# Performance work log

Hardware: AMD Instinct MI355X
Metric: run time of the kernel (lower is better)

Reference implementation:

```python
import jax, jax.numpy as jnp
import numpy as np

B, N, D = 2, 2048, 1024
H, DH = 16, 64
DI = 4096
EPS = 1e-5
NEG_SLOPE = 0.01  # F.leaky_relu default


def _ln(x, g, b):
    mu = jnp.mean(x, axis=-1, keepdims=True)
    var = jnp.mean((x - mu) ** 2, axis=-1, keepdims=True)
    return (x - mu) * jax.lax.rsqrt(var + EPS) * g + b


def setup_inputs() -> dict:
    key = jax.random.key(0)
    ks = jax.random.split(key, 10)
    s = 0.02
    return {
        "Z": jax.random.normal(ks[0], (B, N, D), jnp.float32),
        "new_mask": jax.random.normal(ks[1], (B, N, N), jnp.float32),
        "mask": jax.random.uniform(ks[2], (B, N, N), jnp.float32),
        "ln1_g": jnp.ones((D,), jnp.float32),
        "ln1_b": jnp.zeros((D,), jnp.float32),
        "qkv_w": jax.random.normal(ks[3], (3 * D, D), jnp.float32) * s,
        "qkv_b": jnp.zeros((3 * D,), jnp.float32),
        "o_w": jax.random.normal(ks[4], (D, H * DH), jnp.float32) * s,
        "ln2_g": jnp.ones((D,), jnp.float32),
        "ln2_b": jnp.zeros((D,), jnp.float32),
        "p1_w": jax.random.normal(ks[5], (DI, D), jnp.float32) * s,
        "p1_b": jnp.zeros((DI,), jnp.float32),
        "p2_w": jax.random.normal(ks[6], (D, DI), jnp.float32) * s,
        "p2_b": jnp.zeros((D,), jnp.float32),
    }


def reference(Z, new_mask, mask, ln1_g, ln1_b, qkv_w, qkv_b, o_w, ln2_g, ln2_b, p1_w, p1_b, p2_w, p2_b):
    inp = Z
    Zn = _ln(Z, ln1_g, ln1_b)
    qkv = (Zn @ qkv_w.T + qkv_b).reshape(B, N, H, 3 * DH)
    # torch chunk order in the source: V, Q, K
    V, Q, K = jnp.split(qkv, 3, axis=3)  # each [B,N,H,DH]
    # scores: einsum('bnij,bmij->binm') == [B,H,N,N]
    W = jnp.einsum("bnhd,bmhd->bhnm", Q, K) / np.sqrt(DH) + new_mask[:, None]
    A = jax.nn.softmax(W, axis=3) * mask[:, None]
    attn = jnp.einsum("bhnm,bmhd->bnhd", A, V).reshape(B, N, D)
    attn = jnp.where(attn >= 0, attn, NEG_SLOPE * attn) @ o_w.T  # leaky_relu then o_net (no bias)
    Z1 = attn + inp
    Zn2 = _ln(Z1, ln2_g, ln2_b)
    h = jax.nn.relu(Zn2 @ p1_w.T + p1_b)
    return h @ p2_w.T + p2_b + Z1
```

## Files before the change

kernel.cpp:

```cpp
#include <hip/hip_runtime.h>

typedef unsigned short u16;
typedef __attribute__((ext_vector_type(8))) short bf16x8;
typedef __attribute__((ext_vector_type(2))) float f32x2;
typedef __attribute__((ext_vector_type(4))) float f32x4;
typedef __attribute__((ext_vector_type(16))) float f32x16;
typedef __attribute__((ext_vector_type(4))) unsigned u32x4;

#define DEV static __device__ __forceinline__

DEV u16 f2bf(float f) {
    unsigned u = __float_as_uint(f);
    u += 0x7FFFu + ((u >> 16) & 1u);
    return (u16)(u >> 16);
}

DEV float uaf(unsigned u) { return __uint_as_float(u); }

typedef const __attribute__((address_space(1))) void* gas1_t;
typedef __attribute__((address_space(3))) void* gas3_t;

DEV void gl_lds16(const u16* g, u16* l) {
    __builtin_amdgcn_global_load_lds((gas1_t)g, (gas3_t)l, 16, 0, 0);
}

DEV unsigned cvtpk_bf16(float a, float b) {
    unsigned r;
    asm("v_cvt_pk_bf16_f32 %0, %1, %2" : "=v"(r) : "v"(a), "v"(b));
    return r;
}

DEV int sw8(int row, int chunk) { return row * 64 + ((chunk ^ (row & 7)) << 3); }

__global__ __launch_bounds__(256) void prep_all(const float* __restrict__ qkv_w,
                                                const float* __restrict__ o_w,
                                                const float* __restrict__ p1_w,
                                                const float* __restrict__ p2_w,
                                                const float* __restrict__ qkv_b,
                                                const float* __restrict__ nm,
                                                const float* __restrict__ pm,
                                                const float* __restrict__ Z,
                                                const float* __restrict__ ln1_g,
                                                const float* __restrict__ ln1_b,
                                                u16* __restrict__ qkvW,
                                                u16* __restrict__ oW,
                                                u16* __restrict__ p1W,
                                                u16* __restrict__ p2W,
                                                float* __restrict__ pbias,
                                                unsigned* __restrict__ Mp,
                                                u16* __restrict__ Zn) {
    __shared__ uint4 Ls[512];
    __shared__ float rs[4], rss[4];
    const int bid = blockIdx.x, t = threadIdx.x;
    if (bid < 3072) {
        int i = bid * 256 + t;
        int orow = i >> 8, cc = i & 255;
        int region = orow >> 10, rem = orow & 1023, h = rem >> 6, tt = rem & 63;
        int srow = h * 192 + region * 64 + tt;
        float4 v = ((const float4*)qkv_w)[srow * 256 + cc];
        ushort4 o;
        o.x = f2bf(v.x); o.y = f2bf(v.y); o.z = f2bf(v.z); o.w = f2bf(v.w);
        ((ushort4*)qkvW)[i] = o;
    } else if (bid < 4096) {
        int i = (bid - 3072) * 256 + t;
        float4 v = ((const float4*)o_w)[i];
        ushort4 o;
        o.x = f2bf(v.x); o.y = f2bf(v.y); o.z = f2bf(v.z); o.w = f2bf(v.w);
        ((ushort4*)oW)[i] = o;
    } else if (bid < 8192) {
        int i = (bid - 4096) * 256 + t;
        float4 v = ((const float4*)p1_w)[i];
        ushort4 o;
        o.x = f2bf(v.x); o.y = f2bf(v.y); o.z = f2bf(v.z); o.w = f2bf(v.w);
        ((ushort4*)p1W)[i] = o;
    } else if (bid < 12288) {
        int i = (bid - 8192) * 256 + t;
        float4 v = ((const float4*)p2_w)[i];
        ushort4 o;
        o.x = f2bf(v.x); o.y = f2bf(v.y); o.z = f2bf(v.z); o.w = f2bf(v.w);
        ((ushort4*)p2W)[i] = o;
    } else if (bid < 16384) {
        const int idx = bid - 12288;
        const int bb = idx >> 11, r2 = idx & 2047;
        const int mt = r2 >> 5, nt = r2 & 31;
        const int n0 = nt * 64;
        const int n = t >> 2;
        const int mq0 = (t & 3) * 2;
        const size_t fbase = (size_t)bb * 1048576 + (size_t)(n0 + n) * 512 + mt * 8 + mq0;
        const float4 a0 = ((const float4*)nm)[fbase];
        const float4 a1 = ((const float4*)nm)[fbase + 1];
        const float4 b0 = ((const float4*)pm)[fbase];
        const float4 b1 = ((const float4*)pm)[fbase + 1];
        uint4 o0, o1;
        o0.x = ((unsigned)f2bf(b0.x) << 16) | f2bf(a0.x * 1.4426950f);
        o0.y = ((unsigned)f2bf(b0.y) << 16) | f2bf(a0.y * 1.4426950f);
        o0.z = ((unsigned)f2bf(b0.z) << 16) | f2bf(a0.z * 1.4426950f);
        o0.w = ((unsigned)f2bf(b0.w) << 16) | f2bf(a0.w * 1.4426950f);
        o1.x = ((unsigned)f2bf(b1.x) << 16) | f2bf(a1.x * 1.4426950f);
        o1.y = ((unsigned)f2bf(b1.y) << 16) | f2bf(a1.y * 1.4426950f);
        o1.z = ((unsigned)f2bf(b1.z) << 16) | f2bf(a1.z * 1.4426950f);
        o1.w = ((unsigned)f2bf(b1.w) << 16) | f2bf(a1.w * 1.4426950f);
        const int c = mq0 >> 1;
        Ls[c * 128 + n * 2 + 0] = o0;
        Ls[c * 128 + n * 2 + 1] = o1;
        __syncthreads();
        const int wc = t >> 6, j = t & 63;
        const size_t obase = (((size_t)(bb * 64 + mt) * 4) + wc) * 4096 + (size_t)n0 * 2;
        ((uint4*)Mp)[obase + j] = Ls[wc * 128 + j];
        ((uint4*)Mp)[obase + 64 + j] = Ls[wc * 128 + 64 + j];
    } else if (bid < 20480) {
        const int row = bid - 16384;
        const float4 v = ((const float4*)(Z + (size_t)row * 1024))[t];
        float s = v.x + v.y + v.z + v.w;
        float ss = v.x * v.x + v.y * v.y + v.z * v.z + v.w * v.w;
#pragma unroll
        for (int o = 1; o < 64; o <<= 1) {
            s += __shfl_xor(s, o);
            ss += __shfl_xor(ss, o);
        }
        const int wave = t >> 6, lane = t & 63;
        if (lane == 0) { rs[wave] = s; rss[wave] = ss; }
        __syncthreads();
        const float tot = rs[0] + rs[1] + rs[2] + rs[3];
        const float totss = rss[0] + rss[1] + rss[2] + rss[3];
        const float mu = tot * (1.0f / 1024.0f);
        const float var = totss * (1.0f / 1024.0f) - mu * mu;
        const float rstd = rsqrtf(var + 1e-5f);
        const float4 g4 = ((const float4*)ln1_g)[t];
        const float4 b4 = ((const float4*)ln1_b)[t];
        ushort4 o;
        o.x = f2bf((v.x - mu) * rstd * g4.x + b4.x);
        o.y = f2bf((v.y - mu) * rstd * g4.y + b4.y);
        o.z = f2bf((v.z - mu) * rstd * g4.z + b4.z);
        o.w = f2bf((v.w - mu) * rstd * g4.w + b4.w);
        ((ushort4*)(Zn + (size_t)row * 1024))[t] = o;
    } else {
#pragma unroll
        for (int k = 0; k < 12; k++) {
            int i = k * 256 + t;
            int region = i >> 10, rem = i & 1023, h = rem >> 6, tt = rem & 63;
            pbias[i] = qkv_b[h * 192 + region * 64 + tt];
        }
    }
}

__global__ __launch_bounds__(256) void ln2_comb2(const float* __restrict__ p0,
                                                 const float* __restrict__ p1,
                                                 const float* __restrict__ Z,
                                                 const float* __restrict__ gam,
                                                 const float* __restrict__ bet,
                                                 float* __restrict__ Z1,
                                                 u16* __restrict__ y) {
    const int row = blockIdx.x;
    const int t = threadIdx.x;
    const size_t off = (size_t)row * 256 + t;
    const float4 a = ((const float4*)p0)[off];
    const float4 c = ((const float4*)p1)[off];
    const float4 z = ((const float4*)Z)[off];
    float4 v;
    v.x = a.x + c.x + z.x;
    v.y = a.y + c.y + z.y;
    v.z = a.z + c.z + z.z;
    v.w = a.w + c.w + z.w;
    ((float4*)Z1)[off] = v;
    float s = v.x + v.y + v.z + v.w;
    float ss = v.x * v.x + v.y * v.y + v.z * v.z + v.w * v.w;
#pragma unroll
    for (int o = 1; o < 64; o <<= 1) {
        s += __shfl_xor(s, o);
        ss += __shfl_xor(ss, o);
    }
    __shared__ float rs[4], rss[4];
    const int wave = t >> 6, lane = t & 63;
    if (lane == 0) { rs[wave] = s; rss[wave] = ss; }
    __syncthreads();
    const float tot = rs[0] + rs[1] + rs[2] + rs[3];
    const float totss = rss[0] + rss[1] + rss[2] + rss[3];
    const float mu = tot * (1.0f / 1024.0f);
    const float var = totss * (1.0f / 1024.0f) - mu * mu;
    const float rstd = rsqrtf(var + 1e-5f);
    const float4 g4 = ((const float4*)gam)[t];
    const float4 b4 = ((const float4*)bet)[t];
    ushort4 o;
    o.x = f2bf((v.x - mu) * rstd * g4.x + b4.x);
    o.y = f2bf((v.y - mu) * rstd * g4.y + b4.y);
    o.z = f2bf((v.z - mu) * rstd * g4.z + b4.z);
    o.w = f2bf((v.w - mu) * rstd * g4.w + b4.w);
    ((ushort4*)(y + (size_t)row * 1024))[t] = o;
}

__global__ __launch_bounds__(256) void out_comb(const float* __restrict__ p0,
                                                const float* __restrict__ p1,
                                                const float* __restrict__ bias,
                                                const float* __restrict__ Z1,
                                                float* __restrict__ out) {
    int i = blockIdx.x * 256 + threadIdx.x;
    float4 a = ((const float4*)p0)[i];
    float4 c = ((const float4*)p1)[i];
    float4 z = ((const float4*)Z1)[i];
    float4 b = ((const float4*)bias)[i & 255];
    float4 o;
    o.x = a.x + c.x + z.x + b.x; o.y = a.y + c.y + z.y + b.y;
    o.z = a.z + c.z + z.z + b.z; o.w = a.w + c.w + z.w + b.w;
    ((float4*)out)[i] = o;
}

template <int EPI>
__global__ __launch_bounds__(256, 3) void gemm_bt(const u16* __restrict__ A,
                                                  const u16* __restrict__ Bt,
                                                  const float* __restrict__ bias,
                                                  void* __restrict__ out0,
                                                  void* __restrict__ out1,
                                                  void* __restrict__ out2,
                                                  int M, int N, int K, int ldk) {
    __shared__ __align__(16) u16 As[2][128 * 32];
    __shared__ __align__(16) u16 Bs[2][128 * 32];
    const int tid = threadIdx.x;
    const int wave = tid >> 6, lane = tid & 63;
    const int lhi = lane >> 4, llo = lane & 15;
    const int gx = gridDim.x;
    const int bid = blockIdx.y * gx + blockIdx.x;
    const int swz = (bid & 7) * ((gx * gridDim.y) >> 3) + (bid >> 3);
    const int bx = swz % gx, by = swz / gx;
    const int kz = blockIdx.z * K;

    const int arow = wave * 32 + (lane >> 2);
    const int asw = ((lane & 3) ^ ((lane >> 2) & 3)) << 3;
    const u16* gA = A + (size_t)(by * 128 + arow) * ldk + kz + asw;
    const u16* gB = Bt + (size_t)(bx * 128 + arow) * ldk + kz + asw;
    u16* lA0 = As[0] + wave * 1024 + lane * 8;
    u16* lA1 = As[1] + wave * 1024 + lane * 8;
    u16* lB0 = Bs[0] + wave * 1024 + lane * 8;
    u16* lB1 = Bs[1] + wave * 1024 + lane * 8;

#define GSTAGE(LA, LB) do { \
        gl_lds16(gA, LA); gl_lds16(gA + 16 * (size_t)ldk, (LA) + 512); \
        gl_lds16(gB, LB); gl_lds16(gB + 16 * (size_t)ldk, (LB) + 512); \
        gA += 32; gB += 32; } while (0)

    const int wr = wave >> 1, wc = wave & 1;
    const f32x4 zero = {0.f, 0.f, 0.f, 0.f};
    f32x4 acc[4][4];
#pragma unroll
    for (int i = 0; i < 4; i++)
#pragma unroll
        for (int j = 0; j < 4; j++) acc[i][j] = zero;

#define GPHASE(AB, BB, DO_REFILL, LA, LB, LASTWAIT) do { \
        if (LASTWAIT) asm volatile("s_waitcnt vmcnt(0)" ::: "memory"); \
        else          asm volatile("s_waitcnt vmcnt(4)" ::: "memory"); \
        __builtin_amdgcn_s_barrier(); \
        bf16x8 af[4], bfr[4]; \
        _Pragma("unroll") \
        for (int i = 0; i < 4; i++) { \
            const int r = wr * 64 + i * 16 + llo; \
            af[i] = *(const bf16x8*)((AB) + r * 32 + (((lhi ^ r) & 3) << 3)); \
        } \
        _Pragma("unroll") \
        for (int j = 0; j < 4; j++) { \
            const int r = wc * 64 + j * 16 + llo; \
            bfr[j] = *(const bf16x8*)((BB) + r * 32 + (((lhi ^ r) & 3) << 3)); \
        } \
        asm volatile("s_waitcnt lgkmcnt(0)" ::: "memory"); \
        __builtin_amdgcn_sched_barrier(0); \
        __builtin_amdgcn_s_barrier(); \
        if (DO_REFILL) GSTAGE(LA, LB); \
        __builtin_amdgcn_s_setprio(1); \
        _Pragma("unroll") \
        for (int i = 0; i < 4; i++) \
            _Pragma("unroll") \
            for (int j = 0; j < 4; j++) \
                acc[i][j] = __builtin_amdgcn_mfma_f32_16x16x32_bf16(af[i], bfr[j], acc[i][j], 0, 0, 0); \
        __builtin_amdgcn_s_setprio(0); \
        } while (0)

    GSTAGE(lA0, lB0);
    GSTAGE(lA1, lB1);
    for (int k0 = 0; k0 < K; k0 += 64) {
        const bool r0 = (k0 + 64 < K);
        const bool r1 = (k0 + 96 < K);
        GPHASE(As[0], Bs[0], r0, lA0, lB0, false);
        GPHASE(As[1], Bs[1], r1, lA1, lB1, !r0);
    }
#undef GPHASE
#undef GSTAGE

    const int rbase = by * 128 + wr * 64 + lhi * 4;
    const int cbase = bx * 128 + wc * 64 + llo;
    float* pout = nullptr;
    if constexpr (EPI == 4) {
        pout = (float*)out0 + (size_t)blockIdx.z * M * N;
    }
#pragma unroll
    for (int i = 0; i < 4; i++) {
#pragma unroll
        for (int j = 0; j < 4; j++) {
#pragma unroll
            for (int r = 0; r < 4; r++) {
                const int row = rbase + i * 16 + r;
                const int col = cbase + j * 16;
                float v = acc[i][j][r];
                if constexpr (EPI == 0) {
                    v += bias[col];
                    const int region = col >> 10;
                    const int c = col & 1023;
                    const int b = row >> 11, n = row & 2047;
                    if (region == 0) {
                        ((float*)out0)[(size_t)row * 1024 + c] = v;
                    } else {
                        const int h = c >> 6, t = c & 63;
                        u16* dst = (region == 1) ? (u16*)out1 : (u16*)out2;
                        dst[(((size_t)(b * 16 + h)) * 2048 + n) * 64 + t] = f2bf(v);
                    }
                } else if constexpr (EPI == 2) {
                    v += bias[col];
                    v = v > 0.f ? v : 0.f;
                    ((u16*)out0)[(size_t)row * N + col] = f2bf(v);
                } else {
                    pout[(size_t)row * N + col] = v;
                }
            }
        }
    }
}

__global__ __launch_bounds__(256) void vtrans(const float* __restrict__ Vsc,
                                              u16* __restrict__ Vt) {
    __shared__ u16 Ts[64 * 72];
    const int nt = blockIdx.x;
    const int bh = blockIdx.y;
    const int b = bh >> 4, h = bh & 15;
    const int t = threadIdx.x;
    const int n0 = nt * 64;
    const int nr = t >> 2;
    const int dq = (t & 3) * 16;
    const float* src = Vsc + ((size_t)(b * 2048 + n0 + nr)) * 1024 + h * 64 + dq;
    float4 v0 = ((const float4*)src)[0];
    float4 v1 = ((const float4*)src)[1];
    float4 v2 = ((const float4*)src)[2];
    float4 v3 = ((const float4*)src)[3];
    u16* c0 = Ts + nr;
    c0[(dq + 0) * 72]  = f2bf(v0.x); c0[(dq + 1) * 72]  = f2bf(v0.y);
    c0[(dq + 2) * 72]  = f2bf(v0.z); c0[(dq + 3) * 72]  = f2bf(v0.w);
    c0[(dq + 4) * 72]  = f2bf(v1.x); c0[(dq + 5) * 72]  = f2bf(v1.y);
    c0[(dq + 6) * 72]  = f2bf(v1.z); c0[(dq + 7) * 72]  = f2bf(v1.w);
    c0[(dq + 8) * 72]  = f2bf(v2.x); c0[(dq + 9) * 72]  = f2bf(v2.y);
    c0[(dq + 10) * 72] = f2bf(v2.z); c0[(dq + 11) * 72] = f2bf(v2.w);
    c0[(dq + 12) * 72] = f2bf(v3.x); c0[(dq + 13) * 72] = f2bf(v3.y);
    c0[(dq + 14) * 72] = f2bf(v3.z); c0[(dq + 15) * 72] = f2bf(v3.w);
    __syncthreads();
    const int d = t >> 2, n8 = (t & 3) * 16;
    u16* dstrow = Vt + ((size_t)bh * 64 + d) * 2048 + n0;
#pragma unroll
    for (int w = 0; w < 4; w++) {
        const int gi = (n8 >> 2) + w;
        const int g5 = gi & 7, blk = gi >> 3;
        const int pg = (g5 & 4) | ((g5 & 1) << 1) | ((g5 >> 1) & 1);
        *(uint2*)(dstrow + blk * 32 + pg * 4) = *(const uint2*)(Ts + d * 72 + n8 + w * 4);
    }
}

__global__ __launch_bounds__(256, 4) void attn_fused8(const u16* __restrict__ Qg,
                                                      const u16* __restrict__ Kg,
                                                      const u16* __restrict__ Vtg,
                                                      const unsigned* __restrict__ Mp,
                                                      u16* __restrict__ attnL) {
    __shared__ __align__(16) u16 Ks[2][64 * 64];
    __shared__ __align__(16) u16 Vs[2][64 * 64];
    __shared__ float lsh[2][32], lsh2[2][32];
    const int tid = threadIdx.x, wave = tid >> 6, lane = tid & 63;
    const int qh = wave & 1, wm = wave >> 1;
    const int hi = lane >> 5, l31 = lane & 31;
    const int pid = blockIdx.x;
    const int seq = pid >> 3;
    const int hh = seq & 15;
    const int g = (pid & 7) + (seq >> 4) * 8;
    const int b = g >> 5, qt = g & 31;
    const int bh = b * 16 + hh;
    const int q0 = qt * 64;

    const int l3 = lane >> 3, l7 = lane & 7;
    const int swcol = (l7 ^ l3) << 3;
    const int srow = wave * 16 + l3;
    const u16* kp = Kg + ((size_t)bh * 2048 + srow) * 64 + swcol;
    const u16* vp = Vtg + ((size_t)bh * 64 + srow) * 2048 + swcol;
    u16* lKa = Ks[0] + wave * 1024 + lane * 8;
    u16* lKb = Ks[1] + wave * 1024 + lane * 8;
    u16* lVa = Vs[0] + wave * 1024 + lane * 8;
    u16* lVb = Vs[1] + wave * 1024 + lane * 8;

#define STAGE(LK, LV) do { \
        gl_lds16(kp, LK); gl_lds16(kp + 512, (LK) + 512); \
        gl_lds16(vp, LV); gl_lds16(vp + 16384, (LV) + 512); \
        kp += 4096; vp += 64; } while (0)

    STAGE(lKa, lVa);
    const int qrow = q0 + qh * 32 + l31;
    const u16* qptr = Qg + ((size_t)bh * 2048 + qrow) * 64 + hi * 8;
    bf16x8 qf[4];
#pragma unroll
    for (int ks = 0; ks < 4; ks++) qf[ks] = *(const bf16x8*)(qptr + ks * 16);

    const uint4* mp = (const uint4*)Mp + (size_t)(b * 64 + wm) * 16384
                                       + (size_t)qrow * 2 + hi;

    const f32x16 z16 = {0.f,0.f,0.f,0.f,0.f,0.f,0.f,0.f,0.f,0.f,0.f,0.f,0.f,0.f,0.f,0.f};
    f32x16 accO[2];
    accO[0] = z16; accO[1] = z16;
    f32x2 lsv = {0.f, 0.f};
    const float CS = 0.125f * 1.4426950f;
    const f32x2 csv = {CS, CS};
    __syncthreads();

#define QUAD(M, q) { \
        f32x2 nm0 = {uaf(M.x << 16), uaf(M.y << 16)}; \
        f32x2 nm1 = {uaf(M.z << 16), uaf(M.w << 16)}; \
        const f32x2 sa = {sacc[q], sacc[q + 1]}; \
        const f32x2 sb = {sacc[q + 2], sacc[q + 3]}; \
        nm0 += sa * csv; nm1 += sb * csv; \
        f32x2 e0 = {__builtin_amdgcn_exp2f(nm0.x), __builtin_amdgcn_exp2f(nm0.y)}; \
        f32x2 e1 = {__builtin_amdgcn_exp2f(nm1.x), __builtin_amdgcn_exp2f(nm1.y)}; \
        lsv += e0; lsv += e1; \
        const f32x2 pm0 = {uaf(M.x & 0xFFFF0000u), uaf(M.y & 0xFFFF0000u)}; \
        const f32x2 pm1 = {uaf(M.z & 0xFFFF0000u), uaf(M.w & 0xFFFF0000u)}; \
        e0 *= pm0; e1 *= pm1; \
        wpk[(q) / 2] = cvtpk_bf16(e0.x, e0.y); \
        wpk[(q) / 2 + 1] = cvtpk_bf16(e1.x, e1.y); }

#define ITER(KSB, VSB, LK, LV, DO_STAGE) do { \
        const uint4 M0 = mp[0], M1 = mp[4096], M2 = mp[8192], M3 = mp[12288]; \
        mp += 32768; \
        if (DO_STAGE) STAGE(LK, LV); \
        f32x16 sacc = z16; \
        __builtin_amdgcn_s_setprio(1); \
        _Pragma("unroll") \
        for (int ks = 0; ks < 4; ks++) { \
            const bf16x8 kf = *(const bf16x8*)((KSB) + sw8(wm * 32 + l31, ks * 2 + hi)); \
            sacc = __builtin_amdgcn_mfma_f32_32x32x16_bf16(kf, qf[ks], sacc, 0, 0, 0); \
        } \
        __builtin_amdgcn_s_setprio(0); \
        unsigned wpk[8]; \
        QUAD(M0, 0) QUAD(M1, 4) QUAD(M2, 8) QUAD(M3, 12) \
        const u32x4 fa0v = {wpk[0], wpk[1], wpk[2], wpk[3]}; \
        const u32x4 fa1v = {wpk[4], wpk[5], wpk[6], wpk[7]}; \
        const bf16x8 pa0 = __builtin_bit_cast(bf16x8, fa0v); \
        const bf16x8 pa1 = __builtin_bit_cast(bf16x8, fa1v); \
        __builtin_amdgcn_s_setprio(1); \
        _Pragma("unroll") \
        for (int dh = 0; dh < 2; dh++) { \
            const bf16x8 vf0 = *(const bf16x8*)((VSB) + sw8(dh * 32 + l31, wm * 4 + hi)); \
            accO[dh] = __builtin_amdgcn_mfma_f32_32x32x16_bf16(pa0, vf0, accO[dh], 0, 0, 0); \
            const bf16x8 vf1 = *(const bf16x8*)((VSB) + sw8(dh * 32 + l31, wm * 4 + 2 + hi)); \
            accO[dh] = __builtin_amdgcn_mfma_f32_32x32x16_bf16(pa1, vf1, accO[dh], 0, 0, 0); \
        } \
        __builtin_amdgcn_s_setprio(0); \
        __syncthreads(); } while (0)

    for (int tt = 0; tt < 16; tt++) {
        ITER(Ks[0], Vs[0], lKb, lVb, true);
        ITER(Ks[1], Vs[1], lKa, lVa, (tt < 15));
    }
#undef ITER
#undef QUAD
#undef STAGE

    const float lsum = lsv.x + lsv.y;
    const float lsum2 = lsum + __shfl_xor(lsum, 32);
    float* cb = (float*)&Ks[0][0];
    const int slot = qh * 64 + lane;
    const int s7 = slot & 7;
    if (wm == 1) {
        float* dst = cb + (size_t)slot * 32;
#pragma unroll
        for (int dh = 0; dh < 2; dh++)
#pragma unroll
            for (int c = 0; c < 4; c++) {
                const f32x4 v = {accO[dh][c * 4 + 0], accO[dh][c * 4 + 1],
                                 accO[dh][c * 4 + 2], accO[dh][c * 4 + 3]};
                *(f32x4*)(dst + (((dh * 4 + c) ^ s7) << 2)) = v;
            }
        if (lane < 32) lsh[qh][lane] = lsum2;
    }
    __syncthreads();
    if (wm == 0) {
        const float* src = cb + (size_t)slot * 32;
        const float lt = lsum2 + lsh[qh][l31];
#pragma unroll
        for (int dh = 0; dh < 2; dh++)
#pragma unroll
            for (int c = 0; c < 4; c++) {
                const f32x4 v = *(const f32x4*)(src + (((dh * 4 + c) ^ s7) << 2));
                accO[dh][c * 4 + 0] += v.x;
                accO[dh][c * 4 + 1] += v.y;
                accO[dh][c * 4 + 2] += v.z;
                accO[dh][c * 4 + 3] += v.w;
            }
        if (lane < 32) lsh2[qh][lane] = 1.0f / lt;
    }
    __syncthreads();
    if (wm == 0) {
#pragma unroll
        for (int r = 0; r < 16; r++) {
            const int ql = (r & 3) + 8 * (r >> 2) + 4 * hi;
            const float linv = lsh2[qh][ql];
            const int qg = q0 + qh * 32 + ql;
#pragma unroll
            for (int dh = 0; dh < 2; dh++) {
                float v = accO[dh][r] * linv;
                v = v >= 0.f ? v : 0.01f * v;
                attnL[((size_t)b * 2048 + qg) * 1024 + hh * 64 + dh * 32 + l31] = f2bf(v);
            }
        }
    }
}

extern "C" void kernel_launch(void* const* d_in, const int* in_sizes, int n_in,
                              void* d_out, int out_size, void* d_ws, size_t ws_size,
                              hipStream_t stream) {
    const float* Z     = (const float*)d_in[0];
    const float* nmask = (const float*)d_in[1];
    const float* pmask = (const float*)d_in[2];
    const float* ln1_g = (const float*)d_in[3];
    const float* ln1_b = (const float*)d_in[4];
    const float* qkv_w = (const float*)d_in[5];
    const float* qkv_b = (const float*)d_in[6];
    const float* o_w   = (const float*)d_in[7];
    const float* ln2_g = (const float*)d_in[8];
    const float* ln2_b = (const float*)d_in[9];
    const float* p1_w  = (const float*)d_in[10];
    const float* p1_b  = (const float*)d_in[11];
    const float* p2_w  = (const float*)d_in[12];
    const float* p2_b  = (const float*)d_in[13];
    float* out = (float*)d_out;

    char* w = (char*)d_ws;
    auto take = [&](size_t bytes) -> char* {
        char* p = w;
        w += (bytes + 255) & ~(size_t)255;
        return p;
    };
    u16* qkvW   = (u16*)take((size_t)3072 * 1024 * 2);
    u16* oW     = (u16*)take((size_t)1024 * 1024 * 2);
    u16* p1W    = (u16*)take((size_t)4096 * 1024 * 2);
    u16* p2W    = (u16*)take((size_t)1024 * 4096 * 2);
    u16* Zn     = (u16*)take((size_t)4096 * 1024 * 2);
    u16* Qb     = (u16*)take((size_t)32 * 2048 * 64 * 2);
    u16* Kb     = (u16*)take((size_t)32 * 2048 * 64 * 2);
    u16* Vt     = (u16*)take((size_t)32 * 64 * 2048 * 2);
    u16* attnL  = (u16*)take((size_t)4096 * 1024 * 2);
    float* Z1   = (float*)take((size_t)4096 * 1024 * 4);
    u16* hbuf   = (u16*)take((size_t)4096 * 4096 * 2);
    unsigned* Mp = (unsigned*)take((size_t)2 * 2048 * 2048 * 4);
    float* pbias = (float*)take((size_t)3072 * 4);
    float* Vsc    = (float*)hbuf;
    float* part01 = (float*)Mp;
    float* part23 = (float*)hbuf;

    prep_all<<<dim3(20481), 256, 0, stream>>>(qkv_w, o_w, p1_w, p2_w, qkv_b, nmask, pmask,
                                              Z, ln1_g, ln1_b,
                                              qkvW, oW, p1W, p2W, pbias, Mp, Zn);
    gemm_bt<0><<<dim3(24, 32), 256, 0, stream>>>(Zn, qkvW, pbias, Vsc, Qb, Kb, 4096, 3072, 1024, 1024);
    vtrans<<<dim3(32, 32), 256, 0, stream>>>(Vsc, Vt);
    attn_fused8<<<dim3(1024), 256, 0, stream>>>(Qb, Kb, Vt, Mp, attnL);
    gemm_bt<4><<<dim3(8, 32, 2), 256, 0, stream>>>(attnL, oW, nullptr, part01, nullptr, nullptr,
                                                   4096, 1024, 512, 1024);
    ln2_comb2<<<dim3(4096), 256, 0, stream>>>(part01, part01 + (size_t)4096 * 1024,
                                              Z, ln2_g, ln2_b, Z1, Zn);
    gemm_bt<2><<<dim3(32, 32), 256, 0, stream>>>(Zn, p1W, p1_b, hbuf, nullptr, nullptr,
                                                 4096, 4096, 1024, 1024);
    gemm_bt<4><<<dim3(8, 32, 2), 256, 0, stream>>>(hbuf, p2W, nullptr, part01, nullptr, nullptr,
                                                   4096, 1024, 2048, 4096);
    out_comb<<<dim3(4096), 256, 0, stream>>>(part01, part01 + (size_t)4096 * 1024, p2_b, Z1, out);
}
```

Baseline: 407.6 us.

## Prefetch mask tiles one iteration ahead and fold additive mask into MFMA accumulator

The attention kernel now loads the packed mask tile for the next key block one iteration early, using double-buffered registers, so global-load latency overlaps the current block's compute. The additive mask is pre-scaled by 8 in the prep kernel and written into the score accumulator as its initial value, so the MFMA adds it for free. The whole sum is then multiplied by the combined softmax and log2e scale before exp2. This adds register pressure from the extra 16 mask words held per thread, and changes bf16 rounding of the mask because it is stored scaled by 8 instead of by log2e.

```diff
diff --git a/kernel.cpp b/kernel.cpp
--- a/kernel.cpp
+++ b/kernel.cpp
@@ -92,14 +92,14 @@
         const float4 b0 = ((const float4*)pm)[fbase];
         const float4 b1 = ((const float4*)pm)[fbase + 1];
         uint4 o0, o1;
-        o0.x = ((unsigned)f2bf(b0.x) << 16) | f2bf(a0.x * 1.4426950f);
-        o0.y = ((unsigned)f2bf(b0.y) << 16) | f2bf(a0.y * 1.4426950f);
-        o0.z = ((unsigned)f2bf(b0.z) << 16) | f2bf(a0.z * 1.4426950f);
-        o0.w = ((unsigned)f2bf(b0.w) << 16) | f2bf(a0.w * 1.4426950f);
-        o1.x = ((unsigned)f2bf(b1.x) << 16) | f2bf(a1.x * 1.4426950f);
-        o1.y = ((unsigned)f2bf(b1.y) << 16) | f2bf(a1.y * 1.4426950f);
-        o1.z = ((unsigned)f2bf(b1.z) << 16) | f2bf(a1.z * 1.4426950f);
-        o1.w = ((unsigned)f2bf(b1.w) << 16) | f2bf(a1.w * 1.4426950f);
+        o0.x = ((unsigned)f2bf(b0.x) << 16) | f2bf(a0.x * 8.0f);
+        o0.y = ((unsigned)f2bf(b0.y) << 16) | f2bf(a0.y * 8.0f);
+        o0.z = ((unsigned)f2bf(b0.z) << 16) | f2bf(a0.z * 8.0f);
+        o0.w = ((unsigned)f2bf(b0.w) << 16) | f2bf(a0.w * 8.0f);
+        o1.x = ((unsigned)f2bf(b1.x) << 16) | f2bf(a1.x * 8.0f);
+        o1.y = ((unsigned)f2bf(b1.y) << 16) | f2bf(a1.y * 8.0f);
+        o1.z = ((unsigned)f2bf(b1.z) << 16) | f2bf(a1.z * 8.0f);
+        o1.w = ((unsigned)f2bf(b1.w) << 16) | f2bf(a1.w * 8.0f);
         const int c = mq0 >> 1;
         Ls[c * 128 + n * 2 + 0] = o0;
         Ls[c * 128 + n * 2 + 1] = o1;
@@ -360,7 +360,7 @@
     }
 }
 
-__global__ __launch_bounds__(256, 4) void attn_fused8(const u16* __restrict__ Qg,
+__global__ __launch_bounds__(256, 4) void attn_fused9(const u16* __restrict__ Qg,
                                                       const u16* __restrict__ Kg,
                                                       const u16* __restrict__ Vtg,
                                                       const unsigned* __restrict__ Mp,
@@ -403,6 +403,9 @@
 
     const uint4* mp = (const uint4*)Mp + (size_t)(b * 64 + wm) * 16384
                                        + (size_t)qrow * 2 + hi;
+    uint4 mA0 = mp[0], mA1 = mp[4096], mA2 = mp[8192], mA3 = mp[12288];
+    uint4 mB0, mB1, mB2, mB3;
+    mp += 32768;
 
     const f32x16 z16 = {0.f,0.f,0.f,0.f,0.f,0.f,0.f,0.f,0.f,0.f,0.f,0.f,0.f,0.f,0.f,0.f};
     f32x16 accO[2];
@@ -413,13 +416,10 @@
     __syncthreads();
 
 #define QUAD(M, q) { \
-        f32x2 nm0 = {uaf(M.x << 16), uaf(M.y << 16)}; \
-        f32x2 nm1 = {uaf(M.z << 16), uaf(M.w << 16)}; \
-        const f32x2 sa = {sacc[q], sacc[q + 1]}; \
-        const f32x2 sb = {sacc[q + 2], sacc[q + 3]}; \
-        nm0 += sa * csv; nm1 += sb * csv; \
-        f32x2 e0 = {__builtin_amdgcn_exp2f(nm0.x), __builtin_amdgcn_exp2f(nm0.y)}; \
-        f32x2 e1 = {__builtin_amdgcn_exp2f(nm1.x), __builtin_amdgcn_exp2f(nm1.y)}; \
+        const f32x2 s0 = {sacc[q] * CS, sacc[q + 1] * CS}; \
+        const f32x2 s1 = {sacc[q + 2] * CS, sacc[q + 3] * CS}; \
+        f32x2 e0 = {__builtin_amdgcn_exp2f(s0.x), __builtin_amdgcn_exp2f(s0.y)}; \
+        f32x2 e1 = {__builtin_amdgcn_exp2f(s1.x), __builtin_amdgcn_exp2f(s1.y)}; \
         lsv += e0; lsv += e1; \
         const f32x2 pm0 = {uaf(M.x & 0xFFFF0000u), uaf(M.y & 0xFFFF0000u)}; \
         const f32x2 pm1 = {uaf(M.z & 0xFFFF0000u), uaf(M.w & 0xFFFF0000u)}; \
@@ -427,11 +427,21 @@
         wpk[(q) / 2] = cvtpk_bf16(e0.x, e0.y); \
         wpk[(q) / 2 + 1] = cvtpk_bf16(e1.x, e1.y); }
 
-#define ITER(KSB, VSB, LK, LV, DO_STAGE) do { \
-        const uint4 M0 = mp[0], M1 = mp[4096], M2 = mp[8192], M3 = mp[12288]; \
-        mp += 32768; \
-        if (DO_STAGE) STAGE(LK, LV); \
-        f32x16 sacc = z16; \
+#define ITER(KSB, VSB, LK, LV, MC0, MC1, MC2, MC3, MN0, MN1, MN2, MN3, DO_PF) do { \
+        if (DO_PF) { \
+            MN0 = mp[0]; MN1 = mp[4096]; MN2 = mp[8192]; MN3 = mp[12288]; \
+            mp += 32768; \
+            STAGE(LK, LV); \
+        } \
+        f32x16 sacc; \
+        sacc[0] = uaf(MC0.x << 16); sacc[1] = uaf(MC0.y << 16); \
+        sacc[2] = uaf(MC0.z << 16); sacc[3] = uaf(MC0.w << 16); \
+        sacc[4] = uaf(MC1.x << 16); sacc[5] = uaf(MC1.y << 16); \
+        sacc[6] = uaf(MC1.z << 16); sacc[7] = uaf(MC1.w << 16); \
+        sacc[8] = uaf(MC2.x << 16); sacc[9] = uaf(MC2.y << 16); \
+        sacc[10] = uaf(MC2.z << 16); sacc[11] = uaf(MC2.w << 16); \
+        sacc[12] = uaf(MC3.x << 16); sacc[13] = uaf(MC3.y << 16); \
+        sacc[14] = uaf(MC3.z << 16); sacc[15] = uaf(MC3.w << 16); \
         __builtin_amdgcn_s_setprio(1); \
         _Pragma("unroll") \
         for (int ks = 0; ks < 4; ks++) { \
@@ -440,7 +450,7 @@
         } \
         __builtin_amdgcn_s_setprio(0); \
         unsigned wpk[8]; \
-        QUAD(M0, 0) QUAD(M1, 4) QUAD(M2, 8) QUAD(M3, 12) \
+        QUAD(MC0, 0) QUAD(MC1, 4) QUAD(MC2, 8) QUAD(MC3, 12) \
         const u32x4 fa0v = {wpk[0], wpk[1], wpk[2], wpk[3]}; \
         const u32x4 fa1v = {wpk[4], wpk[5], wpk[6], wpk[7]}; \
         const bf16x8 pa0 = __builtin_bit_cast(bf16x8, fa0v); \
@@ -457,8 +467,8 @@
         __syncthreads(); } while (0)
 
     for (int tt = 0; tt < 16; tt++) {
-        ITER(Ks[0], Vs[0], lKb, lVb, true);
-        ITER(Ks[1], Vs[1], lKa, lVa, (tt < 15));
+        ITER(Ks[0], Vs[0], lKb, lVb, mA0, mA1, mA2, mA3, mB0, mB1, mB2, mB3, true);
+        ITER(Ks[1], Vs[1], lKa, lVa, mB0, mB1, mB2, mB3, mA0, mA1, mA2, mA3, (tt < 15));
     }
 #undef ITER
 #undef QUAD
@@ -561,7 +571,7 @@
                                               qkvW, oW, p1W, p2W, pbias, Mp, Zn);
     gemm_bt<0><<<dim3(24, 32), 256, 0, stream>>>(Zn, qkvW, pbias, Vsc, Qb, Kb, 4096, 3072, 1024, 1024);
     vtrans<<<dim3(32, 32), 256, 0, stream>>>(Vsc, Vt);
-    attn_fused8<<<dim3(1024), 256, 0, stream>>>(Qb, Kb, Vt, Mp, attnL);
+    attn_fused9<<<dim3(1024), 256, 0, stream>>>(Qb, Kb, Vt, Mp, attnL);
     gemm_bt<4><<<dim3(8, 32, 2), 256, 0, stream>>>(attnL, oW, nullptr, part01, nullptr, nullptr,
                                                    4096, 1024, 512, 1024);
     ln2_comb2<<<dim3(4096), 256, 0, stream>>>(part01, part01 + (size_t)4096 * 1024,
```

After: 453.2 us. +11.2%, slower.

## Fuse V transpose into QKV GEMM epilogue via LDS-staged bf16 stores

Applied to the files above, without the earlier changes.

The QKV GEMM epilogue now writes the V region straight into the transposed, permuted bf16 Vt layout. It stages the tile through the reused LDS buffers with an XOR swizzle and then does 16-byte coalesced stores. This removes the separate vtrans kernel and the fp32 Vsc round trip through global memory. The cost is extra barriers and LDS traffic in the V blocks' epilogue, plus a divergent epilogue path between V blocks and Q/K blocks.

```diff
diff --git a/kernel.cpp b/kernel.cpp
--- a/kernel.cpp
+++ b/kernel.cpp
@@ -213,8 +213,7 @@
                                                   void* __restrict__ out1,
                                                   void* __restrict__ out2,
                                                   int M, int N, int K, int ldk) {
-    __shared__ __align__(16) u16 As[2][128 * 32];
-    __shared__ __align__(16) u16 Bs[2][128 * 32];
+    __shared__ __align__(16) u16 SH[4][128 * 32];
     const int tid = threadIdx.x;
     const int wave = tid >> 6, lane = tid & 63;
     const int lhi = lane >> 4, llo = lane & 15;
@@ -228,10 +227,10 @@
     const int asw = ((lane & 3) ^ ((lane >> 2) & 3)) << 3;
     const u16* gA = A + (size_t)(by * 128 + arow) * ldk + kz + asw;
     const u16* gB = Bt + (size_t)(bx * 128 + arow) * ldk + kz + asw;
-    u16* lA0 = As[0] + wave * 1024 + lane * 8;
-    u16* lA1 = As[1] + wave * 1024 + lane * 8;
-    u16* lB0 = Bs[0] + wave * 1024 + lane * 8;
-    u16* lB1 = Bs[1] + wave * 1024 + lane * 8;
+    u16* lA0 = SH[0] + wave * 1024 + lane * 8;
+    u16* lA1 = SH[1] + wave * 1024 + lane * 8;
+    u16* lB0 = SH[2] + wave * 1024 + lane * 8;
+    u16* lB1 = SH[3] + wave * 1024 + lane * 8;
 
 #define GSTAGE(LA, LB) do { \
         gl_lds16(gA, LA); gl_lds16(gA + 16 * (size_t)ldk, (LA) + 512); \
@@ -279,84 +278,93 @@
     for (int k0 = 0; k0 < K; k0 += 64) {
         const bool r0 = (k0 + 64 < K);
         const bool r1 = (k0 + 96 < K);
-        GPHASE(As[0], Bs[0], r0, lA0, lB0, false);
-        GPHASE(As[1], Bs[1], r1, lA1, lB1, !r0);
+        GPHASE(SH[0], SH[2], r0, lA0, lB0, false);
+        GPHASE(SH[1], SH[3], r1, lA1, lB1, !r0);
     }
 #undef GPHASE
 #undef GSTAGE
 
     const int rbase = by * 128 + wr * 64 + lhi * 4;
     const int cbase = bx * 128 + wc * 64 + llo;
-    float* pout = nullptr;
-    if constexpr (EPI == 4) {
-        pout = (float*)out0 + (size_t)blockIdx.z * M * N;
-    }
-#pragma unroll
-    for (int i = 0; i < 4; i++) {
-#pragma unroll
-        for (int j = 0; j < 4; j++) {
-#pragma unroll
-            for (int r = 0; r < 4; r++) {
-                const int row = rbase + i * 16 + r;
-                const int col = cbase + j * 16;
-                float v = acc[i][j][r];
-                if constexpr (EPI == 0) {
-                    v += bias[col];
-                    const int region = col >> 10;
-                    const int c = col & 1023;
-                    const int b = row >> 11, n = row & 2047;
-                    if (region == 0) {
-                        ((float*)out0)[(size_t)row * 1024 + c] = v;
+    if constexpr (EPI == 0) {
+        if (cbase < 1024) {
+            __syncthreads();
+            u16* T = &SH[0][0];
+#pragma unroll
+            for (int i = 0; i < 4; i++) {
+#pragma unroll
+                for (int r = 0; r < 4; r++) {
+                    const int nl = wr * 64 + lhi * 4 + i * 16 + r;
+                    const int g5 = (nl >> 2) & 7;
+                    const int pg = (g5 & 4) | ((g5 & 1) << 1) | ((g5 >> 1) & 1);
+                    const int slot = (nl & ~31) | (pg << 2) | (nl & 3);
+#pragma unroll
+                    for (int j = 0; j < 4; j++) {
+                        const int d = llo + j * 16;
+                        const float v = acc[i][j][r] + bias[cbase + j * 16];
+                        T[wc * 8192 + d * 128 +
+                          ((((slot >> 3) ^ d) & 15) << 3) + (slot & 7)] = f2bf(v);
+                    }
+                }
+            }
+            __syncthreads();
+            const int rowid = tid >> 1, half = tid & 1;
+            const int h2 = rowid >> 6, dd = rowid & 63;
+            const int bb2 = by >> 4;
+            const int nb = (by & 15) * 128;
+            const int headg = bx * 2 + h2;
+            u16* dst = (u16*)out0 + ((size_t)(bb2 * 16 + headg) * 64 + dd) * 2048
+                                  + nb + half * 64;
+            const u16* srcT = T + h2 * 8192 + dd * 128;
+#pragma unroll
+            for (int k = 0; k < 8; k++) {
+                const int grp = half * 8 + k;
+                ((uint4*)dst)[k] = *(const uint4*)(srcT + (((grp ^ dd) & 15) << 3));
+            }
+        } else {
+#pragma unroll
+            for (int i = 0; i < 4; i++) {
+#pragma unroll
+                for (int j = 0; j < 4; j++) {
+#pragma unroll
+                    for (int r = 0; r < 4; r++) {
+                        const int row = rbase + i * 16 + r;
+                        const int col = cbase + j * 16;
+                        const float v = acc[i][j][r] + bias[col];
+                        const int region = col >> 10;
+                        const int c = col & 1023;
+                        const int b = row >> 11, n = row & 2047;
+                        const int h = c >> 6, t2 = c & 63;
+                        u16* dst = (region == 1) ? (u16*)out1 : (u16*)out2;
+                        dst[(((size_t)(b * 16 + h)) * 2048 + n) * 64 + t2] = f2bf(v);
+                    }
+                }
+            }
+        }
+    } else {
+        float* pout = nullptr;
+        if constexpr (EPI == 4) {
+            pout = (float*)out0 + (size_t)blockIdx.z * M * N;
+        }
+#pragma unroll
+        for (int i = 0; i < 4; i++) {
+#pragma unroll
+            for (int j = 0; j < 4; j++) {
+#pragma unroll
+                for (int r = 0; r < 4; r++) {
+                    const int row = rbase + i * 16 + r;
+                    const int col = cbase + j * 16;
+                    float v = acc[i][j][r];
+                    if constexpr (EPI == 2) {
+                        v += bias[col];
+                        v = v > 0.f ? v : 0.f;
+                        ((u16*)out0)[(size_t)row * N + col] = f2bf(v);
                     } else {
-                        const int h = c >> 6, t = c & 63;
-                        u16* dst = (region == 1) ? (u16*)out1 : (u16*)out2;
-                        dst[(((size_t)(b * 16 + h)) * 2048 + n) * 64 + t] = f2bf(v);
+                        pout[(size_t)row * N + col] = v;
                     }
-                } else if constexpr (EPI == 2) {
-                    v += bias[col];
-                    v = v > 0.f ? v : 0.f;
-                    ((u16*)out0)[(size_t)row * N + col] = f2bf(v);
-                } else {
-                    pout[(size_t)row * N + col] = v;
                 }
             }
         }
-    }
-}
-
-__global__ __launch_bounds__(256) void vtrans(const float* __restrict__ Vsc,
-                                              u16* __restrict__ Vt) {
-    __shared__ u16 Ts[64 * 72];
-    const int nt = blockIdx.x;
-    const int bh = blockIdx.y;
-    const int b = bh >> 4, h = bh & 15;
-    const int t = threadIdx.x;
-    const int n0 = nt * 64;
-    const int nr = t >> 2;
-    const int dq = (t & 3) * 16;
-    const float* src = Vsc + ((size_t)(b * 2048 + n0 + nr)) * 1024 + h * 64 + dq;
-    float4 v0 = ((const float4*)src)[0];
-    float4 v1 = ((const float4*)src)[1];
-    float4 v2 = ((const float4*)src)[2];
-    float4 v3 = ((const float4*)src)[3];
-    u16* c0 = Ts + nr;
-    c0[(dq + 0) * 72]  = f2bf(v0.x); c0[(dq + 1) * 72]  = f2bf(v0.y);
-    c0[(dq + 2) * 72]  = f2bf(v0.z); c0[(dq + 3) * 72]  = f2bf(v0.w);
-    c0[(dq + 4) * 72]  = f2bf(v1.x); c0[(dq + 5) * 72]  = f2bf(v1.y);
-    c0[(dq + 6) * 72]  = f2bf(v1.z); c0[(dq + 7) * 72]  = f2bf(v1.w);
-    c0[(dq + 8) * 72]  = f2bf(v2.x); c0[(dq + 9) * 72]  = f2bf(v2.y);
-    c0[(dq + 10) * 72] = f2bf(v2.z); c0[(dq + 11) * 72] = f2bf(v2.w);
-    c0[(dq + 12) * 72] = f2bf(v3.x); c0[(dq + 13) * 72] = f2bf(v3.y);
-    c0[(dq + 14) * 72] = f2bf(v3.z); c0[(dq + 15) * 72] = f2bf(v3.w);
-    __syncthreads();
-    const int d = t >> 2, n8 = (t & 3) * 16;
-    u16* dstrow = Vt + ((size_t)bh * 64 + d) * 2048 + n0;
-#pragma unroll
-    for (int w = 0; w < 4; w++) {
-        const int gi = (n8 >> 2) + w;
-        const int g5 = gi & 7, blk = gi >> 3;
-        const int pg = (g5 & 4) | ((g5 & 1) << 1) | ((g5 >> 1) & 1);
-        *(uint2*)(dstrow + blk * 32 + pg * 4) = *(const uint2*)(Ts + d * 72 + n8 + w * 4);
     }
 }
 
@@ -552,15 +560,12 @@
     u16* hbuf   = (u16*)take((size_t)4096 * 4096 * 2);
     unsigned* Mp = (unsigned*)take((size_t)2 * 2048 * 2048 * 4);
     float* pbias = (float*)take((size_t)3072 * 4);
-    float* Vsc    = (float*)hbuf;
     float* part01 = (float*)Mp;
-    float* part23 = (float*)hbuf;
 
     prep_all<<<dim3(20481), 256, 0, stream>>>(qkv_w, o_w, p1_w, p2_w, qkv_b, nmask, pmask,
                                               Z, ln1_g, ln1_b,
                                               qkvW, oW, p1W, p2W, pbias, Mp, Zn);
-    gemm_bt<0><<<dim3(24, 32), 256, 0, stream>>>(Zn, qkvW, pbias, Vsc, Qb, Kb, 4096, 3072, 1024, 1024);
-    vtrans<<<dim3(32, 32), 256, 0, stream>>>(Vsc, Vt);
+    gemm_bt<0><<<dim3(24, 32), 256, 0, stream>>>(Zn, qkvW, pbias, Vt, Qb, Kb, 4096, 3072, 1024, 1024);
     attn_fused8<<<dim3(1024), 256, 0, stream>>>(Qb, Kb, Vt, Mp, attnL);
     gemm_bt<4><<<dim3(8, 32, 2), 256, 0, stream>>>(attnL, oW, nullptr, part01, nullptr, nullptr,
                                                    4096, 1024, 512, 1024);
```

New measurement: 410.6 us. Within noise of the previous version (+0.8%).
